# Kernel optimization log

Measured on AMD Instinct MI355X. Metric: run time of the kernel, lower is better.

Reference implementation:

```python
import jax, jax.numpy as jnp
import numpy as np

E = 8        # num experts
TOP = 2      # top-k
D = 1024     # emb_size


def setup_inputs() -> dict:
    key = jax.random.key(0)
    ks = jax.random.split(key, 8)
    s = 1.0 / np.sqrt(D)
    x = jax.random.normal(ks[0], (4, 2048, D), dtype=jnp.float32)
    Wg = jax.random.uniform(ks[1], (D, E), jnp.float32, -s, s)
    bg = jax.random.uniform(ks[2], (E,), jnp.float32, -s, s)
    W1 = jax.random.uniform(ks[3], (E, D, D), jnp.float32, -s, s)
    b1 = jax.random.uniform(ks[4], (E, D), jnp.float32, -s, s)
    W2 = jax.random.uniform(ks[5], (E, D, D), jnp.float32, -s, s)
    b2 = jax.random.uniform(ks[6], (E, D), jnp.float32, -s, s)
    return {"x": x, "Wg": Wg, "bg": bg, "W1": W1, "b1": b1, "W2": W2, "b2": b2}


def reference(x, Wg, bg, W1, b1, W2, b2):
    x_shape = x.shape
    xt = x.reshape(-1, x_shape[-1])                       # [N, D] tokens
    gate_prob = jax.nn.softmax(xt @ Wg + bg, axis=-1)     # [N, E]
    top_w, top_i = jax.lax.top_k(gate_prob, TOP)          # [N, TOP]
    top_w = jax.nn.softmax(top_w, axis=-1)                # renormalize over top-k
    N = xt.shape[0]
    # combine weights scattered into dense [N, E] (each token has TOP nonzeros)
    comb = jnp.zeros((N, E), xt.dtype).at[jnp.arange(N)[:, None], top_i].add(top_w)
    # per-expert 2-layer MLP applied to all tokens; masked-out tokens get 0 combine weight
    h = jax.nn.relu(jnp.einsum('nd,edf->enf', xt, W1) + b1[:, None, :])   # [E, N, D]
    ye = jnp.einsum('enf,efg->eng', h, W2) + b2[:, None, :]               # [E, N, D]
    y = jnp.einsum('ne,eng->ng', comb, ye)                                # [N, D]
    return y.reshape(x_shape), gate_prob
```

## Files before the change

### kernel.cpp

```cpp
#include <hip/hip_runtime.h>
#include <stdint.h>

#define TOKENS 8192
#define DIM    1024
#define NEXP   8
#define NASSIGN (TOKENS*2)
#define BK     64
#define NKT    (DIM/BK)

#define C_ROW   16
#define C_TILE  25
#define C_TOTAL 34

#define WS_CTRL  0
#define WS_TOPE  1024
#define WS_TOPW  (WS_TOPE + NASSIGN*4)
#define WS_PTOK  (WS_TOPW + NASSIGN*4)
#define WS_AROW  (WS_PTOK + NASSIGN*4)
#define WS_XB    (WS_AROW + NASSIGN*4)
#define WS_W1T   (WS_XB  + (size_t)TOKENS*DIM*2)
#define WS_W2T   (WS_W1T + (size_t)NEXP*DIM*DIM*2)
#define WS_H     (WS_W2T + (size_t)NEXP*DIM*DIM*2)
#define WS_YE    WS_XB

#define WGLD (DIM + 4)

typedef __attribute__((ext_vector_type(8))) short short8;
typedef __attribute__((ext_vector_type(4))) float floatx4;

__device__ __forceinline__ uint32_t bfr(float f) {
  uint32_t v = __float_as_uint(f);
  return (v + 0x7FFFu + ((v >> 16) & 1u)) >> 16;
}
__device__ __forceinline__ float b2f(uint32_t u) { return __uint_as_float(u << 16); }

__device__ __forceinline__ void load_lds16(const void* g, void* l) {
  __builtin_amdgcn_global_load_lds(
      (const __attribute__((address_space(1))) uint32_t*)g,
      (__attribute__((address_space(3))) uint32_t*)l, 16, 0, 0);
}

__global__ __launch_bounds__(256) void prep_kernel(
    const float* __restrict__ x, const float* __restrict__ Wg,
    const float* __restrict__ bg, float* __restrict__ gate_out,
    int* __restrict__ top_e, float* __restrict__ top_w,
    uint16_t* __restrict__ xb,
    const float* __restrict__ W1, const float* __restrict__ W2,
    uint16_t* __restrict__ W1T, uint16_t* __restrict__ W2T) {
  __shared__ __align__(16) char smem[NEXP * WGLD * 4];
  int t = threadIdx.x;

  if (blockIdx.x >= 2048) {
    uint16_t (*tile)[68] = (uint16_t (*)[68])smem;
    int cb = blockIdx.x - 2048;
    int m  = cb >> 8;
    int d0 = ((cb >> 4) & 15) * 64, f0 = (cb & 15) * 64;
    const float* src = (m < 8) ? (W1 + (size_t)m*DIM*DIM) : (W2 + (size_t)(m-8)*DIM*DIM);
    uint16_t*    dst = (m < 8) ? (W1T + (size_t)m*DIM*DIM) : (W2T + (size_t)(m-8)*DIM*DIM);
    int col = t & 63, rb = (t >> 6) * 16;
    #pragma unroll
    for (int i = 0; i < 16; i++) {
      int dr = rb + i;
      tile[dr][col] = (uint16_t)bfr(src[(size_t)(d0+dr)*DIM + f0 + col]);
    }
    __syncthreads();
    int dg = t & 15, frb = t >> 4;
    #pragma unroll
    for (int i = 0; i < 4; i++) {
      int fr = frb + i * 16;
      uint32_t b0 = tile[dg*4+0][fr], b1 = tile[dg*4+1][fr];
      uint32_t b2 = tile[dg*4+2][fr], b3 = tile[dg*4+3][fr];
      uint2 v;
      v.x = b0 | (b1 << 16);
      v.y = b2 | (b3 << 16);
      *(uint2*)&dst[(size_t)(f0+fr)*DIM + d0 + dg*4] = v;
    }
    return;
  }

  float* wgs = (float*)smem;
  #pragma unroll
  for (int k = 0; k < 32; k++) {
    int i = k * 256 + t;
    float v = Wg[i];
    wgs[(i & 7) * WGLD + (i >> 3)] = v;
  }
  __syncthreads();

  int wave = t >> 6, lane = t & 63;
  int tok = blockIdx.x * 4 + wave;
  const float4* xr = (const float4*)(x + (size_t)tok * DIM);
  uint2* xw = (uint2*)(xb + (size_t)tok * DIM);

  float4 acc[NEXP];
  #pragma unroll
  for (int e = 0; e < NEXP; e++) acc[e] = make_float4(0.f, 0.f, 0.f, 0.f);

  #pragma unroll
  for (int c = 0; c < 4; c++) {
    float4 xv = xr[c * 64 + lane];
    uint2 o;
    o.x = bfr(xv.x) | (bfr(xv.y) << 16);
    o.y = bfr(xv.z) | (bfr(xv.w) << 16);
    xw[c * 64 + lane] = o;
    int d0 = (c * 64 + lane) * 4;
    #pragma unroll
    for (int e = 0; e < NEXP; e++) {
      float4 wv = *(const float4*)&wgs[e * WGLD + d0];
      acc[e].x = fmaf(xv.x, wv.x, acc[e].x);
      acc[e].y = fmaf(xv.y, wv.y, acc[e].y);
      acc[e].z = fmaf(xv.z, wv.z, acc[e].z);
      acc[e].w = fmaf(xv.w, wv.w, acc[e].w);
    }
  }
  float s[NEXP];
  #pragma unroll
  for (int e = 0; e < NEXP; e++) s[e] = (acc[e].x + acc[e].y) + (acc[e].z + acc[e].w);
  #pragma unroll
  for (int off = 32; off > 0; off >>= 1) {
    #pragma unroll
    for (int e = 0; e < NEXP; e++) s[e] += __shfl_xor(s[e], off);
  }
  if (lane == 0) {
    float lg[NEXP], p[NEXP];
    float mx = -1e30f;
    #pragma unroll
    for (int e = 0; e < NEXP; e++) { lg[e] = s[e] + bg[e]; mx = fmaxf(mx, lg[e]); }
    float sum = 0.f;
    #pragma unroll
    for (int e = 0; e < NEXP; e++) { p[e] = expf(lg[e] - mx); sum += p[e]; }
    float inv = 1.f / sum;
    #pragma unroll
    for (int e = 0; e < NEXP; e++) p[e] *= inv;
    float4* go = (float4*)(gate_out + (size_t)tok * NEXP);
    go[0] = make_float4(p[0], p[1], p[2], p[3]);
    go[1] = make_float4(p[4], p[5], p[6], p[7]);
    int i1 = 0;
    #pragma unroll
    for (int e = 1; e < NEXP; e++) if (p[e] > p[i1]) i1 = e;
    int i2 = (i1 == 0) ? 1 : 0;
    #pragma unroll
    for (int e = 0; e < NEXP; e++) if (e != i1 && p[e] > p[i2]) i2 = e;
    float ev = expf(p[i2] - p[i1]);
    float w1 = 1.f / (1.f + ev), w2 = ev / (1.f + ev);
    top_e[2*tok]   = i1; top_e[2*tok+1] = i2;
    top_w[2*tok]   = w1; top_w[2*tok+1] = w2;
  }
}

__global__ __launch_bounds__(1024) void route_kernel(
    const int* __restrict__ top_e, int* __restrict__ ctrl,
    int* __restrict__ ptok, int* __restrict__ arow) {
  __shared__ int sc[NEXP * 1024];
  __shared__ int scnt[NEXP];
  __shared__ int rowstart[NEXP];
  int t = threadIdx.x;
  int e_loc[16];
  int cnt[NEXP];
  #pragma unroll
  for (int e = 0; e < NEXP; e++) cnt[e] = 0;
  #pragma unroll
  for (int j = 0; j < 16; j++) {
    int e = top_e[t * 16 + j];
    e_loc[j] = e;
    cnt[e]++;
  }
  #pragma unroll
  for (int e = 0; e < NEXP; e++) sc[e * 1024 + t] = cnt[e];
  __syncthreads();
  int wave = t >> 6, lane = t & 63;
  if (wave < NEXP) {
    int running = 0;
    for (int chunk = 0; chunk < 16; chunk++) {
      int idx = wave * 1024 + chunk * 64 + lane;
      int v = sc[idx];
      int incl = v;
      #pragma unroll
      for (int off = 1; off < 64; off <<= 1) {
        int u = __shfl_up(incl, off);
        if (lane >= off) incl += u;
      }
      sc[idx] = running + incl - v;
      running += __shfl(incl, 63);
    }
    if (lane == 0) scnt[wave] = running;
  }
  __syncthreads();
  if (t == 0) {
    int rs = 0, ts = 0;
    for (int e = 0; e < NEXP; e++) {
      ctrl[C_ROW + e] = rs;
      ctrl[C_TILE + e] = ts;
      rowstart[e] = rs;
      int c = scnt[e];
      rs += c;
      ts += (c + 127) >> 7;
    }
    ctrl[C_ROW + NEXP] = rs;
    ctrl[C_TILE + NEXP] = ts;
    ctrl[C_TOTAL] = ts;
  }
  __syncthreads();
  int off[NEXP];
  #pragma unroll
  for (int e = 0; e < NEXP; e++) off[e] = rowstart[e] + sc[e * 1024 + t];
  #pragma unroll
  for (int j = 0; j < 16; j++) {
    int i = t * 16 + j;
    int e = e_loc[j];
    int pos = off[e]++;
    ptok[pos] = i >> 1;
    arow[i] = pos;
  }
}

__device__ __forceinline__ bool sched_map(const int* ctrl, int bid,
                                          int& mtile, int& n0) {
  int total = ctrl[C_TOTAL];
  int spx = (total + 7) >> 3;
  int xcd = bid & 7, j = bid >> 3;
  int slot = j >> 3;
  if (slot >= spx) return false;
  mtile = xcd * spx + slot;
  n0 = (j & 7) * 128;
  return mtile < total;
}

__global__ __launch_bounds__(256, 2) void gemm1_kernel(
    const uint16_t* __restrict__ xb, const uint16_t* __restrict__ w1t,
    const float* __restrict__ b1, const int* __restrict__ ctrl,
    const int* __restrict__ ptok, uint16_t* __restrict__ h) {
  __shared__ __align__(16) uint16_t As[2][128*BK];
  __shared__ __align__(16) uint16_t Bs[2][128*BK];
  int mtile, n0;
  if (!sched_map(ctrl, blockIdx.x, mtile, n0)) return;
  int e = 0;
  #pragma unroll
  for (int k = 1; k < NEXP; k++) if (mtile >= ctrl[C_TILE + k]) e = k;
  int row0 = ctrl[C_ROW + e] + (mtile - ctrl[C_TILE + e]) * 128;
  int rend = ctrl[C_ROW + e + 1];

  int t = threadIdx.x, lane = t & 63, w = t >> 6;
  const uint16_t* gA[4];
  const uint16_t* gB[4];
  #pragma unroll
  for (int i = 0; i < 4; i++) {
    int s = i * 256 + t;
    int row = s >> 3, cs = s & 7;
    int gc = cs ^ (row & 7);
    int ar = row0 + row; if (ar > NASSIGN-1) ar = NASSIGN-1;
    int tok = ptok[ar];
    gA[i] = xb  + (size_t)tok * DIM + gc*8;
    gB[i] = w1t + (size_t)e*DIM*DIM + (size_t)(n0 + row)*DIM + gc*8;
  }
  floatx4 acc[4][4];
  #pragma unroll
  for (int mi = 0; mi < 4; mi++)
    #pragma unroll
    for (int ni = 0; ni < 4; ni++) acc[mi][ni] = (floatx4)(0.f);

  int wm = w & 1, wn = w >> 1;
  int l15 = lane & 15, lq = lane >> 4;

  #pragma unroll
  for (int i = 0; i < 4; i++) {
    load_lds16(gA[i], &As[0][(i*256 + t) * 8]);
    load_lds16(gB[i], &Bs[0][(i*256 + t) * 8]);
  }
  for (int kt = 0; kt < NKT; kt++) {
    int cur = kt & 1;
    if (kt + 1 < NKT) {
      #pragma unroll
      for (int i = 0; i < 4; i++) {
        load_lds16(gA[i] + (kt+1)*BK, &As[cur^1][(i*256 + t) * 8]);
        load_lds16(gB[i] + (kt+1)*BK, &Bs[cur^1][(i*256 + t) * 8]);
      }
      asm volatile("s_waitcnt vmcnt(8)" ::: "memory");
    } else {
      asm volatile("s_waitcnt vmcnt(0)" ::: "memory");
    }
    __builtin_amdgcn_s_barrier();
    #pragma unroll
    for (int ks = 0; ks < 2; ks++) {
      short8 a[4], b[4];
      #pragma unroll
      for (int mi = 0; mi < 4; mi++) {
        int row = wm*64 + mi*16 + l15;
        int slot = (ks*4 + lq) ^ (row & 7);
        a[mi] = *(const short8*)&As[cur][row*BK + slot*8];
      }
      #pragma unroll
      for (int ni = 0; ni < 4; ni++) {
        int row = wn*64 + ni*16 + l15;
        int slot = (ks*4 + lq) ^ (row & 7);
        b[ni] = *(const short8*)&Bs[cur][row*BK + slot*8];
      }
      #pragma unroll
      for (int mi = 0; mi < 4; mi++)
        #pragma unroll
        for (int ni = 0; ni < 4; ni++)
          acc[mi][ni] = __builtin_amdgcn_mfma_f32_16x16x32_bf16(a[mi], b[ni], acc[mi][ni], 0, 0, 0);
    }
    __builtin_amdgcn_s_barrier();
  }
  #pragma unroll
  for (int mi = 0; mi < 4; mi++) {
    #pragma unroll
    for (int r = 0; r < 4; r++) {
      int rt = wm*64 + mi*16 + lq*4 + r;
      int ar = row0 + rt;
      if (ar < rend) {
        #pragma unroll
        for (int ni = 0; ni < 4; ni++) {
          int n = n0 + wn*64 + ni*16 + l15;
          float v = acc[mi][ni][r] + b1[e*DIM + n];
          v = fmaxf(v, 0.f);
          h[(size_t)ar*DIM + n] = (uint16_t)bfr(v);
        }
      }
    }
  }
}

__global__ __launch_bounds__(256, 2) void gemm2_kernel(
    const uint16_t* __restrict__ h, const uint16_t* __restrict__ w2t,
    const float* __restrict__ b2, const int* __restrict__ ctrl,
    uint16_t* __restrict__ yeb) {
  __shared__ __align__(16) uint16_t As[2][128*BK];
  __shared__ __align__(16) uint16_t Bs[2][128*BK];
  int mtile, n0;
  if (!sched_map(ctrl, blockIdx.x, mtile, n0)) return;
  int e = 0;
  #pragma unroll
  for (int k = 1; k < NEXP; k++) if (mtile >= ctrl[C_TILE + k]) e = k;
  int row0 = ctrl[C_ROW + e] + (mtile - ctrl[C_TILE + e]) * 128;
  int rend = ctrl[C_ROW + e + 1];

  int t = threadIdx.x, lane = t & 63, w = t >> 6;
  const uint16_t* gA[4];
  const uint16_t* gB[4];
  #pragma unroll
  for (int i = 0; i < 4; i++) {
    int s = i * 256 + t;
    int row = s >> 3, cs = s & 7;
    int gc = cs ^ (row & 7);
    int ar = row0 + row; if (ar > NASSIGN-1) ar = NASSIGN-1;
    gA[i] = h   + (size_t)ar * DIM + gc*8;
    gB[i] = w2t + (size_t)e*DIM*DIM + (size_t)(n0 + row)*DIM + gc*8;
  }
  floatx4 acc[4][4];
  #pragma unroll
  for (int mi = 0; mi < 4; mi++)
    #pragma unroll
    for (int ni = 0; ni < 4; ni++) acc[mi][ni] = (floatx4)(0.f);

  int wm = w & 1, wn = w >> 1;
  int l15 = lane & 15, lq = lane >> 4;

  #pragma unroll
  for (int i = 0; i < 4; i++) {
    load_lds16(gA[i], &As[0][(i*256 + t) * 8]);
    load_lds16(gB[i], &Bs[0][(i*256 + t) * 8]);
  }
  for (int kt = 0; kt < NKT; kt++) {
    int cur = kt & 1;
    if (kt + 1 < NKT) {
      #pragma unroll
      for (int i = 0; i < 4; i++) {
        load_lds16(gA[i] + (kt+1)*BK, &As[cur^1][(i*256 + t) * 8]);
        load_lds16(gB[i] + (kt+1)*BK, &Bs[cur^1][(i*256 + t) * 8]);
      }
      asm volatile("s_waitcnt vmcnt(8)" ::: "memory");
    } else {
      asm volatile("s_waitcnt vmcnt(0)" ::: "memory");
    }
    __builtin_amdgcn_s_barrier();
    #pragma unroll
    for (int ks = 0; ks < 2; ks++) {
      short8 a[4], b[4];
      #pragma unroll
      for (int mi = 0; mi < 4; mi++) {
        int row = wm*64 + mi*16 + l15;
        int slot = (ks*4 + lq) ^ (row & 7);
        a[mi] = *(const short8*)&As[cur][row*BK + slot*8];
      }
      #pragma unroll
      for (int ni = 0; ni < 4; ni++) {
        int row = wn*64 + ni*16 + l15;
        int slot = (ks*4 + lq) ^ (row & 7);
        b[ni] = *(const short8*)&Bs[cur][row*BK + slot*8];
      }
      #pragma unroll
      for (int mi = 0; mi < 4; mi++)
        #pragma unroll
        for (int ni = 0; ni < 4; ni++)
          acc[mi][ni] = __builtin_amdgcn_mfma_f32_16x16x32_bf16(a[mi], b[ni], acc[mi][ni], 0, 0, 0);
    }
    __builtin_amdgcn_s_barrier();
  }
  #pragma unroll
  for (int mi = 0; mi < 4; mi++) {
    #pragma unroll
    for (int r = 0; r < 4; r++) {
      int rt = wm*64 + mi*16 + lq*4 + r;
      int ar = row0 + rt;
      if (ar < rend) {
        #pragma unroll
        for (int ni = 0; ni < 4; ni++) {
          int n = n0 + wn*64 + ni*16 + l15;
          float v = acc[mi][ni][r] + b2[e*DIM + n];
          yeb[(size_t)ar*DIM + n] = (uint16_t)bfr(v);
        }
      }
    }
  }
}

__global__ __launch_bounds__(256) void combine_kernel(
    const uint16_t* __restrict__ yeb, const int* __restrict__ arow,
    const float* __restrict__ top_w, float* __restrict__ y) {
  int t = threadIdx.x;
  int tok = blockIdx.x * 2 + (t >> 7);
  int i = t & 127;
  int r0 = arow[2*tok], r1 = arow[2*tok+1];
  float w0 = top_w[2*tok], w1 = top_w[2*tok+1];
  const uint4* a = (const uint4*)(yeb + (size_t)r0 * DIM);
  const uint4* b = (const uint4*)(yeb + (size_t)r1 * DIM);
  uint4 av = a[i], bv = b[i];
  float4* yo = (float4*)(y + (size_t)tok * DIM + i * 8);
  float4 o0, o1;
  o0.x = w0 * b2f(av.x & 0xFFFFu) + w1 * b2f(bv.x & 0xFFFFu);
  o0.y = w0 * b2f(av.x >> 16)     + w1 * b2f(bv.x >> 16);
  o0.z = w0 * b2f(av.y & 0xFFFFu) + w1 * b2f(bv.y & 0xFFFFu);
  o0.w = w0 * b2f(av.y >> 16)     + w1 * b2f(bv.y >> 16);
  o1.x = w0 * b2f(av.z & 0xFFFFu) + w1 * b2f(bv.z & 0xFFFFu);
  o1.y = w0 * b2f(av.z >> 16)     + w1 * b2f(bv.z >> 16);
  o1.z = w0 * b2f(av.w & 0xFFFFu) + w1 * b2f(bv.w & 0xFFFFu);
  o1.w = w0 * b2f(av.w >> 16)     + w1 * b2f(bv.w >> 16);
  yo[0] = o0;
  yo[1] = o1;
}

extern "C" void kernel_launch(void* const* d_in, const int* in_sizes, int n_in,
                              void* d_out, int out_size, void* d_ws, size_t ws_size,
                              hipStream_t stream) {
  const float* x  = (const float*)d_in[0];
  const float* Wg = (const float*)d_in[1];
  const float* bg = (const float*)d_in[2];
  const float* W1 = (const float*)d_in[3];
  const float* b1 = (const float*)d_in[4];
  const float* W2 = (const float*)d_in[5];
  const float* b2 = (const float*)d_in[6];
  float* out = (float*)d_out;
  char* ws = (char*)d_ws;

  int*      ctrl = (int*)(ws + WS_CTRL);
  int*      tope = (int*)(ws + WS_TOPE);
  float*    topw = (float*)(ws + WS_TOPW);
  int*      ptok = (int*)(ws + WS_PTOK);
  int*      arow = (int*)(ws + WS_AROW);
  uint16_t* xb   = (uint16_t*)(ws + WS_XB);
  uint16_t* w1t  = (uint16_t*)(ws + WS_W1T);
  uint16_t* w2t  = (uint16_t*)(ws + WS_W2T);
  uint16_t* hbuf = (uint16_t*)(ws + WS_H);
  uint16_t* yeb  = (uint16_t*)(ws + WS_YE);

  prep_kernel<<<6144, 256, 0, stream>>>(x, Wg, bg, out + (size_t)TOKENS*DIM,
                                        tope, topw, xb, W1, W2, w1t, w2t);
  route_kernel<<<1, 1024, 0, stream>>>(tope, ctrl, ptok, arow);

  gemm1_kernel<<<136*8, 256, 0, stream>>>(xb, w1t, b1, ctrl, ptok, hbuf);
  gemm2_kernel<<<136*8, 256, 0, stream>>>(hbuf, w2t, b2, ctrl, yeb);
  combine_kernel<<<TOKENS/2, 256, 0, stream>>>(yeb, arow, topw, out);
}
```

Before: 287.5 us.

## Use 128x256 tiles, 512-thread blocks and a 3-stage LDS pipeline in expert GEMMs

Merges the two grouped GEMM kernels into one templated body. It grows the output tile from 128x128 to 128x256 using 8 waves per block. It replaces double buffering with a three-stage LDS ring, so only one barrier is needed per k-step, and raises wave priority around the MFMA section. The aim is better reuse of the A tile across more output columns and deeper hiding of global-load latency. The cost is lower occupancy (one 512-thread block per CU, about 144KB of LDS) and a remapped job schedule across XCDs.

```diff
diff --git a/kernel.cpp b/kernel.cpp
--- a/kernel.cpp
+++ b/kernel.cpp
@@ -7,6 +7,7 @@
 #define NASSIGN (TOKENS*2)
 #define BK     64
 #define NKT    (DIM/BK)
+#define BUF_U16 24576
 
 #define C_ROW   16
 #define C_TILE  25
@@ -68,11 +69,11 @@
     #pragma unroll
     for (int i = 0; i < 4; i++) {
       int fr = frb + i * 16;
-      uint32_t b0 = tile[dg*4+0][fr], b1 = tile[dg*4+1][fr];
-      uint32_t b2 = tile[dg*4+2][fr], b3 = tile[dg*4+3][fr];
+      uint32_t c0 = tile[dg*4+0][fr], c1 = tile[dg*4+1][fr];
+      uint32_t c2 = tile[dg*4+2][fr], c3 = tile[dg*4+3][fr];
       uint2 v;
-      v.x = b0 | (b1 << 16);
-      v.y = b2 | (b3 << 16);
+      v.x = c0 | (c1 << 16);
+      v.y = c2 | (c3 << 16);
       *(uint2*)&dst[(size_t)(f0+fr)*DIM + d0 + dg*4] = v;
     }
     return;
@@ -214,26 +215,20 @@
   }
 }
 
-__device__ __forceinline__ bool sched_map(const int* ctrl, int bid,
-                                          int& mtile, int& n0) {
+template<bool G1>
+__device__ __forceinline__ void gemm_body(
+    const int* ctrl, const int* ptok,
+    const uint16_t* __restrict__ Asrc, const uint16_t* __restrict__ Bsrc,
+    const float* __restrict__ bias, uint16_t* __restrict__ dst,
+    uint16_t* lds) {
   int total = ctrl[C_TOTAL];
-  int spx = (total + 7) >> 3;
-  int xcd = bid & 7, j = bid >> 3;
-  int slot = j >> 3;
-  if (slot >= spx) return false;
-  mtile = xcd * spx + slot;
-  n0 = (j & 7) * 128;
-  return mtile < total;
-}
-
-__global__ __launch_bounds__(256, 2) void gemm1_kernel(
-    const uint16_t* __restrict__ xb, const uint16_t* __restrict__ w1t,
-    const float* __restrict__ b1, const int* __restrict__ ctrl,
-    const int* __restrict__ ptok, uint16_t* __restrict__ h) {
-  __shared__ __align__(16) uint16_t As[2][128*BK];
-  __shared__ __align__(16) uint16_t Bs[2][128*BK];
-  int mtile, n0;
-  if (!sched_map(ctrl, blockIdx.x, mtile, n0)) return;
+  int jobs  = total * 4;
+  int spx   = (jobs + 7) >> 3;
+  int xcd = blockIdx.x & 7, j = blockIdx.x >> 3;
+  if (j >= spx) return;
+  int li = xcd * spx + j;
+  if (li >= jobs) return;
+  int mtile = li >> 2, n0 = (li & 3) * 256;
   int e = 0;
   #pragma unroll
   for (int k = 1; k < NEXP; k++) if (mtile >= ctrl[C_TILE + k]) e = k;
@@ -241,45 +236,59 @@
   int rend = ctrl[C_ROW + e + 1];
 
   int t = threadIdx.x, lane = t & 63, w = t >> 6;
-  const uint16_t* gA[4];
+  int wm = w >> 2, wn = w & 3;
+  int l15 = lane & 15, lq = lane >> 4;
+
+  const uint16_t* gA[2];
   const uint16_t* gB[4];
   #pragma unroll
+  for (int i = 0; i < 2; i++) {
+    int s = i * 512 + t;
+    int row = s >> 3, gc = (s & 7) ^ (row & 7);
+    int ar = row0 + row; if (ar > NASSIGN-1) ar = NASSIGN-1;
+    if (G1) {
+      int tok = ptok[ar];
+      gA[i] = Asrc + (size_t)tok * DIM + gc*8;
+    } else {
+      gA[i] = Asrc + (size_t)ar * DIM + gc*8;
+    }
+  }
+  #pragma unroll
   for (int i = 0; i < 4; i++) {
-    int s = i * 256 + t;
-    int row = s >> 3, cs = s & 7;
-    int gc = cs ^ (row & 7);
-    int ar = row0 + row; if (ar > NASSIGN-1) ar = NASSIGN-1;
-    int tok = ptok[ar];
-    gA[i] = xb  + (size_t)tok * DIM + gc*8;
-    gB[i] = w1t + (size_t)e*DIM*DIM + (size_t)(n0 + row)*DIM + gc*8;
-  }
+    int s = i * 512 + t;
+    int row = s >> 3, gc = (s & 7) ^ (row & 7);
+    gB[i] = Bsrc + (size_t)e*DIM*DIM + (size_t)(n0 + row)*DIM + gc*8;
+  }
+
   floatx4 acc[4][4];
   #pragma unroll
   for (int mi = 0; mi < 4; mi++)
     #pragma unroll
     for (int ni = 0; ni < 4; ni++) acc[mi][ni] = (floatx4)(0.f);
 
-  int wm = w & 1, wn = w >> 1;
-  int l15 = lane & 15, lq = lane >> 4;
-
-  #pragma unroll
-  for (int i = 0; i < 4; i++) {
-    load_lds16(gA[i], &As[0][(i*256 + t) * 8]);
-    load_lds16(gB[i], &Bs[0][(i*256 + t) * 8]);
-  }
+  #pragma unroll
+  for (int p = 0; p < 2; p++) {
+    uint16_t* base = lds + p * BUF_U16;
+    #pragma unroll
+    for (int i = 0; i < 2; i++) { load_lds16(gA[i], base + (size_t)(i*512 + t)*8); gA[i] += BK; }
+    #pragma unroll
+    for (int i = 0; i < 4; i++) { load_lds16(gB[i], base + 8192 + (size_t)(i*512 + t)*8); gB[i] += BK; }
+  }
+
+  #pragma unroll
   for (int kt = 0; kt < NKT; kt++) {
-    int cur = kt & 1;
-    if (kt + 1 < NKT) {
-      #pragma unroll
-      for (int i = 0; i < 4; i++) {
-        load_lds16(gA[i] + (kt+1)*BK, &As[cur^1][(i*256 + t) * 8]);
-        load_lds16(gB[i] + (kt+1)*BK, &Bs[cur^1][(i*256 + t) * 8]);
-      }
-      asm volatile("s_waitcnt vmcnt(8)" ::: "memory");
-    } else {
-      asm volatile("s_waitcnt vmcnt(0)" ::: "memory");
-    }
-    __builtin_amdgcn_s_barrier();
+    if (kt < NKT - 1) asm volatile("s_waitcnt vmcnt(6)\ns_barrier" ::: "memory");
+    else              asm volatile("s_waitcnt vmcnt(0)\ns_barrier" ::: "memory");
+    if (kt + 2 < NKT) {
+      uint16_t* base = lds + ((kt + 2) % 3) * BUF_U16;
+      #pragma unroll
+      for (int i = 0; i < 2; i++) { load_lds16(gA[i], base + (size_t)(i*512 + t)*8); gA[i] += BK; }
+      #pragma unroll
+      for (int i = 0; i < 4; i++) { load_lds16(gB[i], base + 8192 + (size_t)(i*512 + t)*8); gB[i] += BK; }
+    }
+    const uint16_t* pA = lds + (kt % 3) * BUF_U16;
+    const uint16_t* pB = pA + 8192;
+    __builtin_amdgcn_s_setprio(1);
     #pragma unroll
     for (int ks = 0; ks < 2; ks++) {
       short8 a[4], b[4];
@@ -287,13 +296,13 @@
       for (int mi = 0; mi < 4; mi++) {
         int row = wm*64 + mi*16 + l15;
         int slot = (ks*4 + lq) ^ (row & 7);
-        a[mi] = *(const short8*)&As[cur][row*BK + slot*8];
+        a[mi] = *(const short8*)&pA[row*BK + slot*8];
       }
       #pragma unroll
       for (int ni = 0; ni < 4; ni++) {
         int row = wn*64 + ni*16 + l15;
         int slot = (ks*4 + lq) ^ (row & 7);
-        b[ni] = *(const short8*)&Bs[cur][row*BK + slot*8];
+        b[ni] = *(const short8*)&pB[row*BK + slot*8];
       }
       #pragma unroll
       for (int mi = 0; mi < 4; mi++)
@@ -301,8 +310,9 @@
         for (int ni = 0; ni < 4; ni++)
           acc[mi][ni] = __builtin_amdgcn_mfma_f32_16x16x32_bf16(a[mi], b[ni], acc[mi][ni], 0, 0, 0);
     }
-    __builtin_amdgcn_s_barrier();
-  }
+    __builtin_amdgcn_s_setprio(0);
+  }
+
   #pragma unroll
   for (int mi = 0; mi < 4; mi++) {
     #pragma unroll
@@ -313,107 +323,29 @@
         #pragma unroll
         for (int ni = 0; ni < 4; ni++) {
           int n = n0 + wn*64 + ni*16 + l15;
-          float v = acc[mi][ni][r] + b1[e*DIM + n];
-          v = fmaxf(v, 0.f);
-          h[(size_t)ar*DIM + n] = (uint16_t)bfr(v);
+          float v = acc[mi][ni][r] + bias[e*DIM + n];
+          if (G1) v = fmaxf(v, 0.f);
+          dst[(size_t)ar*DIM + n] = (uint16_t)bfr(v);
         }
       }
     }
   }
 }
 
-__global__ __launch_bounds__(256, 2) void gemm2_kernel(
+__global__ __launch_bounds__(512, 1) void gemm1_kernel(
+    const uint16_t* __restrict__ xb, const uint16_t* __restrict__ w1t,
+    const float* __restrict__ b1, const int* __restrict__ ctrl,
+    const int* __restrict__ ptok, uint16_t* __restrict__ h) {
+  __shared__ __align__(16) uint16_t lds[3 * BUF_U16];
+  gemm_body<true>(ctrl, ptok, xb, w1t, b1, h, lds);
+}
+
+__global__ __launch_bounds__(512, 1) void gemm2_kernel(
     const uint16_t* __restrict__ h, const uint16_t* __restrict__ w2t,
     const float* __restrict__ b2, const int* __restrict__ ctrl,
-    uint16_t* __restrict__ yeb) {
-  __shared__ __align__(16) uint16_t As[2][128*BK];
-  __shared__ __align__(16) uint16_t Bs[2][128*BK];
-  int mtile, n0;
-  if (!sched_map(ctrl, blockIdx.x, mtile, n0)) return;
-  int e = 0;
-  #pragma unroll
-  for (int k = 1; k < NEXP; k++) if (mtile >= ctrl[C_TILE + k]) e = k;
-  int row0 = ctrl[C_ROW + e] + (mtile - ctrl[C_TILE + e]) * 128;
-  int rend = ctrl[C_ROW + e + 1];
-
-  int t = threadIdx.x, lane = t & 63, w = t >> 6;
-  const uint16_t* gA[4];
-  const uint16_t* gB[4];
-  #pragma unroll
-  for (int i = 0; i < 4; i++) {
-    int s = i * 256 + t;
-    int row = s >> 3, cs = s & 7;
-    int gc = cs ^ (row & 7);
-    int ar = row0 + row; if (ar > NASSIGN-1) ar = NASSIGN-1;
-    gA[i] = h   + (size_t)ar * DIM + gc*8;
-    gB[i] = w2t + (size_t)e*DIM*DIM + (size_t)(n0 + row)*DIM + gc*8;
-  }
-  floatx4 acc[4][4];
-  #pragma unroll
-  for (int mi = 0; mi < 4; mi++)
-    #pragma unroll
-    for (int ni = 0; ni < 4; ni++) acc[mi][ni] = (floatx4)(0.f);
-
-  int wm = w & 1, wn = w >> 1;
-  int l15 = lane & 15, lq = lane >> 4;
-
-  #pragma unroll
-  for (int i = 0; i < 4; i++) {
-    load_lds16(gA[i], &As[0][(i*256 + t) * 8]);
-    load_lds16(gB[i], &Bs[0][(i*256 + t) * 8]);
-  }
-  for (int kt = 0; kt < NKT; kt++) {
-    int cur = kt & 1;
-    if (kt + 1 < NKT) {
-      #pragma unroll
-      for (int i = 0; i < 4; i++) {
-        load_lds16(gA[i] + (kt+1)*BK, &As[cur^1][(i*256 + t) * 8]);
-        load_lds16(gB[i] + (kt+1)*BK, &Bs[cur^1][(i*256 + t) * 8]);
-      }
-      asm volatile("s_waitcnt vmcnt(8)" ::: "memory");
-    } else {
-      asm volatile("s_waitcnt vmcnt(0)" ::: "memory");
-    }
-    __builtin_amdgcn_s_barrier();
-    #pragma unroll
-    for (int ks = 0; ks < 2; ks++) {
-      short8 a[4], b[4];
-      #pragma unroll
-      for (int mi = 0; mi < 4; mi++) {
-        int row = wm*64 + mi*16 + l15;
-        int slot = (ks*4 + lq) ^ (row & 7);
-        a[mi] = *(const short8*)&As[cur][row*BK + slot*8];
-      }
-      #pragma unroll
-      for (int ni = 0; ni < 4; ni++) {
-        int row = wn*64 + ni*16 + l15;
-        int slot = (ks*4 + lq) ^ (row & 7);
-        b[ni] = *(const short8*)&Bs[cur][row*BK + slot*8];
-      }
-      #pragma unroll
-      for (int mi = 0; mi < 4; mi++)
-        #pragma unroll
-        for (int ni = 0; ni < 4; ni++)
-          acc[mi][ni] = __builtin_amdgcn_mfma_f32_16x16x32_bf16(a[mi], b[ni], acc[mi][ni], 0, 0, 0);
-    }
-    __builtin_amdgcn_s_barrier();
-  }
-  #pragma unroll
-  for (int mi = 0; mi < 4; mi++) {
-    #pragma unroll
-    for (int r = 0; r < 4; r++) {
-      int rt = wm*64 + mi*16 + lq*4 + r;
-      int ar = row0 + rt;
-      if (ar < rend) {
-        #pragma unroll
-        for (int ni = 0; ni < 4; ni++) {
-          int n = n0 + wn*64 + ni*16 + l15;
-          float v = acc[mi][ni][r] + b2[e*DIM + n];
-          yeb[(size_t)ar*DIM + n] = (uint16_t)bfr(v);
-        }
-      }
-    }
-  }
+    const int* __restrict__ ptok, uint16_t* __restrict__ yeb) {
+  __shared__ __align__(16) uint16_t lds[3 * BUF_U16];
+  gemm_body<false>(ctrl, ptok, h, w2t, b2, yeb, lds);
 }
 
 __global__ __launch_bounds__(256) void combine_kernel(
@@ -468,8 +400,7 @@
   prep_kernel<<<6144, 256, 0, stream>>>(x, Wg, bg, out + (size_t)TOKENS*DIM,
                                         tope, topw, xb, W1, W2, w1t, w2t);
   route_kernel<<<1, 1024, 0, stream>>>(tope, ctrl, ptok, arow);
-
-  gemm1_kernel<<<136*8, 256, 0, stream>>>(xb, w1t, b1, ctrl, ptok, hbuf);
-  gemm2_kernel<<<136*8, 256, 0, stream>>>(hbuf, w2t, b2, ctrl, yeb);
+  gemm1_kernel<<<8*68, 512, 0, stream>>>(xb, w1t, b1, ctrl, ptok, hbuf);
+  gemm2_kernel<<<8*68, 512, 0, stream>>>(hbuf, w2t, b2, ctrl, ptok, yeb);
   combine_kernel<<<TOKENS/2, 256, 0, stream>>>(yeb, arow, topw, out);
 }
```

Result: no change. 285.2 us (-0.8%).
